# Kernel optimization log

Measured on AMD Instinct MI355X. Metric: run time of the kernel, lower is better.

Reference implementation:

```python
import jax, jax.numpy as jnp
import numpy as np

N_NODES = 50000
N_EDGES = 1600000
IN_DIM = 128
OUT_DIM = 32
N_HEADS = 4


def setup_inputs() -> dict:
    key = jax.random.key(0)
    k_x, k_e, k_w, k_a = jax.random.split(key, 4)
    x = jax.random.normal(k_x, (N_NODES, IN_DIM), dtype=jnp.float32)
    edge_index = jax.random.randint(k_e, (N_EDGES, 2), 0, N_NODES, dtype=jnp.int64)
    # Xavier-uniform-like init scales
    w_bound = np.sqrt(6.0 / (IN_DIM + OUT_DIM)).astype(np.float32)
    a_bound = np.sqrt(6.0 / (N_HEADS + 2 * OUT_DIM)).astype(np.float32)
    weight = jax.random.uniform(k_w, (N_HEADS, IN_DIM, OUT_DIM), dtype=jnp.float32,
                                minval=-w_bound, maxval=w_bound)
    attn = jax.random.uniform(k_a, (N_HEADS, 2 * OUT_DIM), dtype=jnp.float32,
                              minval=-a_bound, maxval=a_bound)
    return {"x": x, "edge_index": edge_index, "weight": weight, "attn": attn}


def reference(x, edge_index, weight, attn):
    # x: [N, in_dim]; edge_index: [E, 2]; weight: [H, in, out]; attn: [H, 2*out]
    num_nodes = x.shape[0]
    out_dim = weight.shape[2]
    src = edge_index[:, 0]
    dst = edge_index[:, 1]

    # Per-head linear transform: [N, H, out]
    Wh = jnp.einsum('ni,hio->nho', x, weight)
    Wh_src = Wh[src]  # [E, H, out]
    Wh_dst = Wh[dst]  # [E, H, out]

    a_src = attn[:, :out_dim]   # [H, out]
    a_dst = attn[:, out_dim:]   # [H, out]
    # Edge scores: [E, H]
    e = jnp.einsum('eho,ho->eh', Wh_src, a_src) + jnp.einsum('eho,ho->eh', Wh_dst, a_dst)
    e = jax.nn.leaky_relu(e, negative_slope=0.2)

    # Segment softmax over incoming edges of each dst node
    max_per_dst = jax.ops.segment_max(e, dst, num_segments=num_nodes)  # [N, H]
    max_per_dst = jnp.where(jnp.isfinite(max_per_dst), max_per_dst, 0.0)
    exp_e = jnp.exp(e - max_per_dst[dst])                               # [E, H]
    sum_per_dst = jax.ops.segment_sum(exp_e, dst, num_segments=num_nodes)  # [N, H]
    alpha = exp_e / (sum_per_dst[dst] + 1e-9)                           # [E, H]
    # Dropout is identity in eval mode.

    # Weighted scatter-add aggregation: [N, H, out]
    out = jax.ops.segment_sum(alpha[:, :, None] * Wh_src, dst, num_segments=num_nodes)
    h = out.reshape(num_nodes, -1)  # concat heads -> [N, H*out]
    return h, alpha
```

## Files before the change

kernel.cpp:

```cpp
#include <hip/hip_runtime.h>
#include <hip/hip_bf16.h>
#include <math.h>

#define N_NODES 50000
#define N_EDGES 1600000
#define IN_DIM  128
#define OUT_DIM 32
#define N_HEADS 4
#define WH_DIM  (N_HEADS * OUT_DIM)
#define CAP     128
#define NB_SCAN 196
#define NPASS   4
#define WIN     (N_NODES / NPASS)
#define NCHUNK  32
#define CE      (N_EDGES / NCHUNK)

typedef __attribute__((ext_vector_type(8))) short short8;
typedef __attribute__((ext_vector_type(4))) float floatx4;

__device__ __forceinline__ short f2bf(float v) {
    __hip_bfloat16 b = __float2bfloat16(v);
    return *reinterpret_cast<short*>(&b);
}
__device__ __forceinline__ float lrelu(float v) {
    return v > 0.0f ? v : 0.2f * v;
}

__device__ __forceinline__ void load_edge(const void* eidx, int is32, int e,
                                          int& s, int& d) {
    if (is32) {
        const int2 v = ((const int2*)eidx)[e];
        s = v.x; d = v.y;
    } else {
        const longlong2 v = ((const longlong2*)eidx)[e];
        s = (int)v.x; d = (int)v.y;
    }
}

__global__ __launch_bounds__(256) void k_cvt(
        const void* __restrict__ eidx,
        int* __restrict__ s32, int* __restrict__ d32) {
    __shared__ int s_is32;
    const int t = threadIdx.x;
    if (t < 64) {
        int hi = ((const int*)eidx)[2 * (t * 25000) + 1];
        unsigned long long b = __ballot(hi != 0);
        if (t == 0) s_is32 = (b != 0ULL) ? 1 : 0;
    }
    __syncthreads();
    const int is32 = s_is32;
    const int e = blockIdx.x * 256 + t;
    if (e >= N_EDGES) return;
    int s, d;
    load_edge(eidx, is32, e, s, d);
    s32[e] = s;
    d32[e] = d;
}

__global__ __launch_bounds__(256) void k_wh(
        const float* __restrict__ x, const float* __restrict__ weight,
        const float* __restrict__ attn,
        __hip_bfloat16* __restrict__ Wh16, float* __restrict__ sb16) {
    __shared__ float ubuf[128 * 8];
    __shared__ short xsw[4 * 4 * 64 * 8];
    __shared__ short bsw[4 * 9 * 64 * 8];
    const int t  = threadIdx.x;
    const int nb = blockIdx.x * 64;

    {
        int c = t & 7, k0 = t >> 3;
        int h = c & 3;
        const float* ap = attn + h * 64 + (c >> 2) * 32;
        for (int k = k0; k < 128; k += 32) {
            const float* wp = weight + h * (IN_DIM * OUT_DIM) + k * OUT_DIM;
            float u = 0.f;
#pragma unroll
            for (int o = 0; o < 32; o += 4) {
                float4 wv = *(const float4*)(wp + o);
                float4 av = *(const float4*)(ap + o);
                u += wv.x * av.x + wv.y * av.y + wv.z * av.z + wv.w * av.w;
            }
            ubuf[k * 8 + c] = u;
        }
    }
    __syncthreads();

    for (int f = t; f < 128 * 128; f += 256) {
        int k = f >> 7, c = f & 127;
        float w = weight[(c >> 5) * (IN_DIM * OUT_DIM) + k * OUT_DIM + (c & 31)];
        int kc = k >> 5, quad = (k >> 3) & 3, j = k & 7;
        bsw[((kc * 9 + (c >> 4)) * 64 + quad * 16 + (c & 15)) * 8 + j] = f2bf(w);
    }
    for (int f = t; f < 128 * 16; f += 256) {
        int k = f >> 4, c = f & 15;
        float w = (c < 8) ? ubuf[k * 8 + c] : 0.f;
        int kc = k >> 5, quad = (k >> 3) & 3, j = k & 7;
        bsw[((kc * 9 + 8) * 64 + quad * 16 + c) * 8 + j] = f2bf(w);
    }
    for (int f = t; f < 64 * 32; f += 256) {
        int n = f >> 5, k = (f & 31) * 4;
        int ng = nb + n; if (ng > N_NODES - 1) ng = N_NODES - 1;
        float4 v = *(const float4*)(x + (size_t)ng * IN_DIM + k);
        int wg = n >> 4, m = n & 15, kc = k >> 5, quad = (k >> 3) & 3, j = k & 7;
        short4 sv = make_short4(f2bf(v.x), f2bf(v.y), f2bf(v.z), f2bf(v.w));
        *(short4*)&xsw[(((wg * 4 + kc) * 64) + quad * 16 + m) * 8 + j] = sv;
    }
    __syncthreads();

    const int wg = t >> 6, lane = t & 63;
    floatx4 acc[9];
#pragma unroll
    for (int i = 0; i < 9; ++i) acc[i] = (floatx4){0.f, 0.f, 0.f, 0.f};
#pragma unroll
    for (int kc = 0; kc < 4; ++kc) {
        short8 a = *(short8*)&xsw[((wg * 4 + kc) * 64 + lane) * 8];
#pragma unroll
        for (int cg = 0; cg < 9; ++cg) {
            short8 b = *(short8*)&bsw[((kc * 9 + cg) * 64 + lane) * 8];
            acc[cg] = __builtin_amdgcn_mfma_f32_16x16x32_bf16(a, b, acc[cg],
                                                              0, 0, 0);
        }
    }

    const int col = lane & 15, quad = lane >> 4;
#pragma unroll
    for (int r = 0; r < 4; ++r) {
        int n = nb + wg * 16 + quad * 4 + r;
        if (n >= N_NODES) continue;
#pragma unroll
        for (int cg = 0; cg < 8; ++cg)
            Wh16[(size_t)n * WH_DIM + cg * 16 + col] =
                __float2bfloat16(acc[cg][r]);
        if (col < 8) sb16[(size_t)n * 16 + col] = acc[8][r];
    }
}

__global__ __launch_bounds__(1024) void k_hist(
        const int* __restrict__ d32, int* __restrict__ hist) {
    __shared__ int hbin[WIN];
    const int c = blockIdx.x, w = blockIdx.y;
    for (int i = threadIdx.x; i < WIN; i += 1024) hbin[i] = 0;
    __syncthreads();
    const int w0 = w * WIN;
    for (int e = c * CE + threadIdx.x; e < (c + 1) * CE; e += 1024) {
        unsigned u = (unsigned)(d32[e] - w0);
        if (u < WIN) atomicAdd(&hbin[u], 1);
    }
    __syncthreads();
    for (int i = threadIdx.x; i < WIN; i += 1024)
        hist[c * N_NODES + w0 + i] = hbin[i];
}

__global__ __launch_bounds__(256) void k_scan1(
        const int* __restrict__ hist, int* __restrict__ pre,
        int* __restrict__ bsum) {
    __shared__ int sh[256];
    const int t = threadIdx.x;
    const int i = blockIdx.x * 256 + t;
    int v = 0;
    if (i < N_NODES)
        for (int c = 0; c < NCHUNK; ++c) v += hist[c * N_NODES + i];
    sh[t] = v;
    __syncthreads();
    for (int d = 1; d < 256; d <<= 1) {
        int u = (t >= d) ? sh[t - d] : 0;
        __syncthreads();
        sh[t] += u;
        __syncthreads();
    }
    if (i < N_NODES) pre[i] = sh[t] - v;
    if (t == 255) bsum[blockIdx.x] = sh[255];
}

__global__ __launch_bounds__(256) void k_scan2(
        const int* __restrict__ bsum, int* __restrict__ bbase) {
    __shared__ int sh[256];
    const int t = threadIdx.x;
    int v = (t < NB_SCAN) ? bsum[t] : 0;
    sh[t] = v;
    __syncthreads();
    for (int d = 1; d < 256; d <<= 1) {
        int u = (t >= d) ? sh[t - d] : 0;
        __syncthreads();
        sh[t] += u;
        __syncthreads();
    }
    if (t < NB_SCAN) bbase[t] = sh[t] - v;
}

__global__ __launch_bounds__(256) void k_base(
        const int* __restrict__ pre, const int* __restrict__ bbase,
        int* __restrict__ hist) {
    int d = blockIdx.x * 256 + threadIdx.x;
    if (d >= N_NODES) return;
    int run = pre[d] + bbase[d >> 8];
    for (int c = 0; c < NCHUNK; ++c) {
        int t0 = hist[c * N_NODES + d];
        hist[c * N_NODES + d] = run;
        run += t0;
    }
}

__global__ __launch_bounds__(1024) void k_scatter(
        const int* __restrict__ s32, const int* __restrict__ d32,
        const int* __restrict__ hist, int* __restrict__ csr) {
    __shared__ int pos[WIN];
    const int c = blockIdx.x, w = blockIdx.y;
    const int w0 = w * WIN;
    for (int i = threadIdx.x; i < WIN; i += 1024)
        pos[i] = hist[c * N_NODES + w0 + i];
    __syncthreads();
    for (int e = c * CE + threadIdx.x; e < (c + 1) * CE; e += 1024) {
        unsigned u = (unsigned)(d32[e] - w0);
        if (u < WIN) {
            int p = atomicAdd(&pos[u], 1);
            csr[p] = s32[e];
        }
    }
}

__global__ __launch_bounds__(256) void k_node(
        const int* __restrict__ pre, const int* __restrict__ bbase,
        const int* __restrict__ csr, float* __restrict__ sb16,
        const __hip_bfloat16* __restrict__ Wh16,
        float* __restrict__ out_h) {
    __shared__ int    sbuf[4][CAP];
    __shared__ float4 e4b[4][CAP];
    const int wv = threadIdx.x >> 6;
    const int t  = threadIdx.x & 63;
    const int n  = blockIdx.x * 4 + wv;
    const int beg = pre[n] + bbase[n >> 8];
    const int end = (n + 1 < N_NODES) ? pre[n + 1] + bbase[(n + 1) >> 8]
                                      : N_EDGES;
    const int deg = end - beg;

    const float4 sd = *(const float4*)(sb16 + (size_t)n * 16 + 4);

    float4 sum = {0.f, 0.f, 0.f, 0.f};
    for (int l = t; l < deg; l += 64) {
        int s = csr[beg + l];
        float4 ss = *(const float4*)(sb16 + (size_t)s * 16);
        float4 ex;
        ex.x = __expf(lrelu(ss.x + sd.x));
        ex.y = __expf(lrelu(ss.y + sd.y));
        ex.z = __expf(lrelu(ss.z + sd.z));
        ex.w = __expf(lrelu(ss.w + sd.w));
        if (l < CAP) { sbuf[wv][l] = s; e4b[wv][l] = ex; }
        sum.x += ex.x; sum.y += ex.y; sum.z += ex.z; sum.w += ex.w;
    }
#pragma unroll
    for (int o = 32; o; o >>= 1) {
        sum.x += __shfl_xor(sum.x, o);
        sum.y += __shfl_xor(sum.y, o);
        sum.z += __shfl_xor(sum.z, o);
        sum.w += __shfl_xor(sum.w, o);
    }
    float4 inv;
    inv.x = 1.0f / (sum.x + 1e-9f); inv.y = 1.0f / (sum.y + 1e-9f);
    inv.z = 1.0f / (sum.z + 1e-9f); inv.w = 1.0f / (sum.w + 1e-9f);
    if (t == 0) *(float4*)(sb16 + (size_t)n * 16 + 8) = inv;

    const int esl = t >> 4;
    const int dsl = t & 15;
    const int h   = dsl >> 2;
    const float invh = (h == 0) ? inv.x : (h == 1) ? inv.y
                     : (h == 2) ? inv.z : inv.w;
    const float sdh  = (h == 0) ? sd.x : (h == 1) ? sd.y
                     : (h == 2) ? sd.z : sd.w;
    float acc0 = 0.f, acc1 = 0.f, acc2 = 0.f, acc3 = 0.f;
    float acc4 = 0.f, acc5 = 0.f, acc6 = 0.f, acc7 = 0.f;
    if (deg <= CAP) {
        const int sPad = sbuf[wv][0];
        for (int jb = 0; jb < deg; jb += 16) {
            int   sg[4];
            float ag[4];
#pragma unroll
            for (int g = 0; g < 4; ++g) {
                const int idx = jb + g * 4 + esl;
                sg[g] = sPad;
                ag[g] = 0.f;
                if (idx < deg) {
                    sg[g] = sbuf[wv][idx];
                    ag[g] = ((const float*)&e4b[wv][idx])[h];
                }
            }
            uint4 w0 = *(const uint4*)(Wh16 + (size_t)sg[0] * WH_DIM + dsl * 8);
            uint4 w1 = *(const uint4*)(Wh16 + (size_t)sg[1] * WH_DIM + dsl * 8);
            uint4 w2 = *(const uint4*)(Wh16 + (size_t)sg[2] * WH_DIM + dsl * 8);
            uint4 w3 = *(const uint4*)(Wh16 + (size_t)sg[3] * WH_DIM + dsl * 8);
#define ACC8(W, A)                                                            \
            acc0 += (A) * __uint_as_float((W).x << 16);                       \
            acc1 += (A) * __uint_as_float((W).x & 0xffff0000u);               \
            acc2 += (A) * __uint_as_float((W).y << 16);                       \
            acc3 += (A) * __uint_as_float((W).y & 0xffff0000u);               \
            acc4 += (A) * __uint_as_float((W).z << 16);                       \
            acc5 += (A) * __uint_as_float((W).z & 0xffff0000u);               \
            acc6 += (A) * __uint_as_float((W).w << 16);                       \
            acc7 += (A) * __uint_as_float((W).w & 0xffff0000u)
            ACC8(w0, ag[0]);
            ACC8(w1, ag[1]);
            ACC8(w2, ag[2]);
            ACC8(w3, ag[3]);
#undef ACC8
        }
    } else {
        for (int jb = 0; jb < deg; jb += 4) {
            const int idx = jb + esl;
            float a = 0.f;
            int s = sbuf[wv][0];
            if (idx < deg) {
                if (idx < CAP) {
                    s = sbuf[wv][idx];
                    a = ((const float*)&e4b[wv][idx])[h];
                } else {
                    s = csr[beg + idx];
                    a = __expf(lrelu(sb16[(size_t)s * 16 + h] + sdh));
                }
            }
            const uint4 w = *(const uint4*)(Wh16 + (size_t)s * WH_DIM + dsl * 8);
            acc0 += a * __uint_as_float(w.x << 16);
            acc1 += a * __uint_as_float(w.x & 0xffff0000u);
            acc2 += a * __uint_as_float(w.y << 16);
            acc3 += a * __uint_as_float(w.y & 0xffff0000u);
            acc4 += a * __uint_as_float(w.z << 16);
            acc5 += a * __uint_as_float(w.z & 0xffff0000u);
            acc6 += a * __uint_as_float(w.w << 16);
            acc7 += a * __uint_as_float(w.w & 0xffff0000u);
        }
    }
    acc0 += __shfl_xor(acc0, 16); acc0 += __shfl_xor(acc0, 32);
    acc1 += __shfl_xor(acc1, 16); acc1 += __shfl_xor(acc1, 32);
    acc2 += __shfl_xor(acc2, 16); acc2 += __shfl_xor(acc2, 32);
    acc3 += __shfl_xor(acc3, 16); acc3 += __shfl_xor(acc3, 32);
    acc4 += __shfl_xor(acc4, 16); acc4 += __shfl_xor(acc4, 32);
    acc5 += __shfl_xor(acc5, 16); acc5 += __shfl_xor(acc5, 32);
    acc6 += __shfl_xor(acc6, 16); acc6 += __shfl_xor(acc6, 32);
    acc7 += __shfl_xor(acc7, 16); acc7 += __shfl_xor(acc7, 32);
    if (t < 16) {
        float* op = out_h + (size_t)n * WH_DIM + dsl * 8;
        float4 o0 = {acc0 * invh, acc1 * invh, acc2 * invh, acc3 * invh};
        float4 o1 = {acc4 * invh, acc5 * invh, acc6 * invh, acc7 * invh};
        *(float4*)op = o0;
        *(float4*)(op + 4) = o1;
    }
}

__global__ __launch_bounds__(256) void k_alpha(
        const int* __restrict__ s32, const int* __restrict__ d32,
        const float* __restrict__ sb16, float* __restrict__ ebuf) {
    int e = blockIdx.x * 256 + threadIdx.x;
    if (e >= N_EDGES) return;
    int s = s32[e], d = d32[e];
    float4 ss = *(const float4*)(sb16 + (size_t)s * 16);
    float4 sd = *(const float4*)(sb16 + (size_t)d * 16 + 4);
    float4 iv = *(const float4*)(sb16 + (size_t)d * 16 + 8);
    float4 a;
    a.x = __expf(lrelu(ss.x + sd.x)) * iv.x;
    a.y = __expf(lrelu(ss.y + sd.y)) * iv.y;
    a.z = __expf(lrelu(ss.z + sd.z)) * iv.z;
    a.w = __expf(lrelu(ss.w + sd.w)) * iv.w;
    *(float4*)(ebuf + (size_t)e * 4) = a;
}

extern "C" void kernel_launch(void* const* d_in, const int* in_sizes, int n_in,
                              void* d_out, int out_size, void* d_ws, size_t ws_size,
                              hipStream_t stream) {
    const float* x      = (const float*)d_in[0];
    const void*  eidx   = d_in[1];
    const float* weight = (const float*)d_in[2];
    const float* attn   = (const float*)d_in[3];

    float* out   = (float*)d_out;
    float* out_h = out;
    float* ebuf  = out + (size_t)N_NODES * WH_DIM;

    char* ws = (char*)d_ws;
    int*   bsum  = (int*)(ws + 64);
    int*   bbase = (int*)(ws + 896);
    int*   pre   = (int*)(ws + 2048);
    int*   s32   = (int*)(ws + 202112);
    int*   d32   = (int*)(ws + 6602112);
    int*   hist  = (int*)(ws + 13002112);
    int*   csr   = (int*)(ws + 19402112);
    __hip_bfloat16* Wh16 = (__hip_bfloat16*)(ws + 25802112);
    float* sb16  = (float*)(ws + 38602112);

    k_cvt<<<(N_EDGES + 255) / 256, 256, 0, stream>>>(eidx, s32, d32);
    k_wh<<<(N_NODES + 63) / 64, 256, 0, stream>>>(x, weight, attn, Wh16, sb16);
    dim3 hg(NCHUNK, NPASS);
    k_hist<<<hg, 1024, 0, stream>>>(d32, hist);
    k_scan1<<<NB_SCAN, 256, 0, stream>>>(hist, pre, bsum);
    k_scan2<<<1, 256, 0, stream>>>(bsum, bbase);
    k_base<<<NB_SCAN, 256, 0, stream>>>(pre, bbase, hist);
    k_scatter<<<hg, 1024, 0, stream>>>(s32, d32, hist, csr);
    k_node<<<N_NODES / 4, 256, 0, stream>>>(pre, bbase, csr, sb16,
                                            Wh16, out_h);
    k_alpha<<<(N_EDGES + 255) / 256, 256, 0, stream>>>(s32, d32, sb16, ebuf);
}
```

Baseline: 276.7 us.

## Bucket edges by destination window to avoid redundant full-edge scans in CSR build

The conversion kernel now also partitions edges into per-window buckets using shared and global atomics. Histogram and scatter passes then read only their own window's edges instead of every pass rescanning all edges. The two scan-finalisation kernels are merged, a node offset array is precomputed for the node kernel, and the Wh projection moves after the CSR build so its buffers can alias the bucket storage. In exchange, the conversion kernel writes extra data and relies on a fixed per-window capacity, which assumes roughly uniform destinations.

```diff
diff --git a/kernel.cpp b/kernel.cpp
--- a/kernel.cpp
+++ b/kernel.cpp
@@ -12,8 +12,8 @@
 #define NB_SCAN 196
 #define NPASS   4
 #define WIN     (N_NODES / NPASS)
-#define NCHUNK  32
-#define CE      (N_EDGES / NCHUNK)
+#define NCH2    32
+#define SEGCAP  420000
 
 typedef __attribute__((ext_vector_type(8))) short short8;
 typedef __attribute__((ext_vector_type(4))) float floatx4;
@@ -39,22 +39,35 @@
 
 __global__ __launch_bounds__(256) void k_cvt(
         const void* __restrict__ eidx,
-        int* __restrict__ s32, int* __restrict__ d32) {
+        int* __restrict__ s32, int* __restrict__ d32,
+        int* __restrict__ win_cnt,
+        int* __restrict__ win_s, int* __restrict__ win_d) {
     __shared__ int s_is32;
+    __shared__ int cnt[NPASS];
+    __shared__ int base[NPASS];
     const int t = threadIdx.x;
     if (t < 64) {
         int hi = ((const int*)eidx)[2 * (t * 25000) + 1];
         unsigned long long b = __ballot(hi != 0);
         if (t == 0) s_is32 = (b != 0ULL) ? 1 : 0;
     }
-    __syncthreads();
-    const int is32 = s_is32;
+    if (t < NPASS) cnt[t] = 0;
+    __syncthreads();
     const int e = blockIdx.x * 256 + t;
-    if (e >= N_EDGES) return;
     int s, d;
-    load_edge(eidx, is32, e, s, d);
+    load_edge(eidx, s_is32, e, s, d);
     s32[e] = s;
     d32[e] = d;
+    const int w = d / WIN;
+    const int slot = atomicAdd(&cnt[w], 1);
+    __syncthreads();
+    if (t < NPASS) base[t] = atomicAdd(&win_cnt[t], cnt[t]);
+    __syncthreads();
+    const int p = base[w] + slot;
+    if (p < SEGCAP) {
+        win_s[w * SEGCAP + p] = s;
+        win_d[w * SEGCAP + p] = d;
+    }
 }
 
 __global__ __launch_bounds__(256) void k_wh(
@@ -136,19 +149,24 @@
 }
 
 __global__ __launch_bounds__(1024) void k_hist(
-        const int* __restrict__ d32, int* __restrict__ hist) {
+        const int* __restrict__ win_cnt, const int* __restrict__ win_d,
+        int* __restrict__ hist) {
     __shared__ int hbin[WIN];
     const int c = blockIdx.x, w = blockIdx.y;
     for (int i = threadIdx.x; i < WIN; i += 1024) hbin[i] = 0;
     __syncthreads();
+    const int cw = win_cnt[w];
+    const int ce = (cw + NCH2 - 1) / NCH2;
+    const int lo = c * ce;
+    const int hi = min(lo + ce, cw);
     const int w0 = w * WIN;
-    for (int e = c * CE + threadIdx.x; e < (c + 1) * CE; e += 1024) {
-        unsigned u = (unsigned)(d32[e] - w0);
+    for (int i = lo + threadIdx.x; i < hi; i += 1024) {
+        unsigned u = (unsigned)(win_d[w * SEGCAP + i] - w0);
         if (u < WIN) atomicAdd(&hbin[u], 1);
     }
     __syncthreads();
     for (int i = threadIdx.x; i < WIN; i += 1024)
-        hist[c * N_NODES + w0 + i] = hbin[i];
+        hist[(w * NCH2 + c) * WIN + i] = hbin[i];
 }
 
 __global__ __launch_bounds__(256) void k_scan1(
@@ -158,8 +176,10 @@
     const int t = threadIdx.x;
     const int i = blockIdx.x * 256 + t;
     int v = 0;
-    if (i < N_NODES)
-        for (int c = 0; c < NCHUNK; ++c) v += hist[c * N_NODES + i];
+    if (i < N_NODES) {
+        const int w = i / WIN, bin = i % WIN;
+        for (int c = 0; c < NCH2; ++c) v += hist[(w * NCH2 + c) * WIN + bin];
+    }
     sh[t] = v;
     __syncthreads();
     for (int d = 1; d < 256; d <<= 1) {
@@ -172,8 +192,9 @@
     if (t == 255) bsum[blockIdx.x] = sh[255];
 }
 
-__global__ __launch_bounds__(256) void k_scan2(
-        const int* __restrict__ bsum, int* __restrict__ bbase) {
+__global__ __launch_bounds__(256) void k_base2(
+        const int* __restrict__ bsum, const int* __restrict__ pre,
+        int* __restrict__ hist, int* __restrict__ noff) {
     __shared__ int sh[256];
     const int t = threadIdx.x;
     int v = (t < NB_SCAN) ? bsum[t] : 0;
@@ -185,42 +206,48 @@
         sh[t] += u;
         __syncthreads();
     }
-    if (t < NB_SCAN) bbase[t] = sh[t] - v;
-}
-
-__global__ __launch_bounds__(256) void k_base(
-        const int* __restrict__ pre, const int* __restrict__ bbase,
-        int* __restrict__ hist) {
-    int d = blockIdx.x * 256 + threadIdx.x;
-    if (d >= N_NODES) return;
-    int run = pre[d] + bbase[d >> 8];
-    for (int c = 0; c < NCHUNK; ++c) {
-        int t0 = hist[c * N_NODES + d];
-        hist[c * N_NODES + d] = run;
+    const int b = blockIdx.x;
+    const int exb = sh[b] - bsum[b];
+    if (b == 0 && t == 0) noff[N_NODES] = N_EDGES;
+    const int i = b * 256 + t;
+    if (i >= N_NODES) return;
+    int run = pre[i] + exb;
+    noff[i] = run;
+    const int w = i / WIN, bin = i % WIN;
+    for (int c = 0; c < NCH2; ++c) {
+        const int idx = (w * NCH2 + c) * WIN + bin;
+        int t0 = hist[idx];
+        hist[idx] = run;
         run += t0;
     }
 }
 
 __global__ __launch_bounds__(1024) void k_scatter(
-        const int* __restrict__ s32, const int* __restrict__ d32,
+        const int* __restrict__ win_cnt, const int* __restrict__ win_s,
+        const int* __restrict__ win_d,
         const int* __restrict__ hist, int* __restrict__ csr) {
     __shared__ int pos[WIN];
     const int c = blockIdx.x, w = blockIdx.y;
+    for (int i = threadIdx.x; i < WIN; i += 1024)
+        pos[i] = hist[(w * NCH2 + c) * WIN + i];
+    __syncthreads();
+    const int cw = win_cnt[w];
+    const int ce = (cw + NCH2 - 1) / NCH2;
+    const int lo = c * ce;
+    const int hi = min(lo + ce, cw);
     const int w0 = w * WIN;
-    for (int i = threadIdx.x; i < WIN; i += 1024)
-        pos[i] = hist[c * N_NODES + w0 + i];
-    __syncthreads();
-    for (int e = c * CE + threadIdx.x; e < (c + 1) * CE; e += 1024) {
-        unsigned u = (unsigned)(d32[e] - w0);
+    for (int i = lo + threadIdx.x; i < hi; i += 1024) {
+        int s = win_s[w * SEGCAP + i];
+        unsigned u = (unsigned)(win_d[w * SEGCAP + i] - w0);
         if (u < WIN) {
             int p = atomicAdd(&pos[u], 1);
-            csr[p] = s32[e];
+            csr[p] = s;
         }
     }
 }
 
 __global__ __launch_bounds__(256) void k_node(
-        const int* __restrict__ pre, const int* __restrict__ bbase,
+        const int* __restrict__ noff,
         const int* __restrict__ csr, float* __restrict__ sb16,
         const __hip_bfloat16* __restrict__ Wh16,
         float* __restrict__ out_h) {
@@ -229,9 +256,8 @@
     const int wv = threadIdx.x >> 6;
     const int t  = threadIdx.x & 63;
     const int n  = blockIdx.x * 4 + wv;
-    const int beg = pre[n] + bbase[n >> 8];
-    const int end = (n + 1 < N_NODES) ? pre[n + 1] + bbase[(n + 1) >> 8]
-                                      : N_EDGES;
+    const int beg = noff[n];
+    const int end = noff[n + 1];
     const int deg = end - beg;
 
     const float4 sd = *(const float4*)(sb16 + (size_t)n * 16 + 4);
@@ -375,25 +401,29 @@
     float* ebuf  = out + (size_t)N_NODES * WH_DIM;
 
     char* ws = (char*)d_ws;
-    int*   bsum  = (int*)(ws + 64);
-    int*   bbase = (int*)(ws + 896);
-    int*   pre   = (int*)(ws + 2048);
-    int*   s32   = (int*)(ws + 202112);
-    int*   d32   = (int*)(ws + 6602112);
-    int*   hist  = (int*)(ws + 13002112);
-    int*   csr   = (int*)(ws + 19402112);
-    __hip_bfloat16* Wh16 = (__hip_bfloat16*)(ws + 25802112);
-    float* sb16  = (float*)(ws + 38602112);
-
-    k_cvt<<<(N_EDGES + 255) / 256, 256, 0, stream>>>(eidx, s32, d32);
+    int*   win_cnt = (int*)ws;
+    int*   bsum    = (int*)(ws + 64);
+    int*   pre     = (int*)(ws + 1024);
+    int*   noff    = (int*)(ws + 201024);
+    int*   s32     = (int*)(ws + 401088);
+    int*   d32     = (int*)(ws + 6801088);
+    int*   csr     = (int*)(ws + 13201088);
+    int*   win_s   = (int*)(ws + 19601152);
+    int*   win_d   = (int*)(ws + 26321152);
+    int*   hist    = (int*)(ws + 33041152);
+    __hip_bfloat16* Wh16 = (__hip_bfloat16*)(ws + 19601152);
+    float* sb16    = (float*)(ws + 32401152);
+
+    hipMemsetAsync(win_cnt, 0, 4 * sizeof(int), stream);
+
+    k_cvt<<<N_EDGES / 256, 256, 0, stream>>>(eidx, s32, d32,
+                                             win_cnt, win_s, win_d);
+    dim3 hg(NCH2, NPASS);
+    k_hist<<<hg, 1024, 0, stream>>>(win_cnt, win_d, hist);
+    k_scan1<<<NB_SCAN, 256, 0, stream>>>(hist, pre, bsum);
+    k_base2<<<NB_SCAN, 256, 0, stream>>>(bsum, pre, hist, noff);
+    k_scatter<<<hg, 1024, 0, stream>>>(win_cnt, win_s, win_d, hist, csr);
     k_wh<<<(N_NODES + 63) / 64, 256, 0, stream>>>(x, weight, attn, Wh16, sb16);
-    dim3 hg(NCHUNK, NPASS);
-    k_hist<<<hg, 1024, 0, stream>>>(d32, hist);
-    k_scan1<<<NB_SCAN, 256, 0, stream>>>(hist, pre, bsum);
-    k_scan2<<<1, 256, 0, stream>>>(bsum, bbase);
-    k_base<<<NB_SCAN, 256, 0, stream>>>(pre, bbase, hist);
-    k_scatter<<<hg, 1024, 0, stream>>>(s32, d32, hist, csr);
-    k_node<<<N_NODES / 4, 256, 0, stream>>>(pre, bbase, csr, sb16,
-                                            Wh16, out_h);
+    k_node<<<N_NODES / 4, 256, 0, stream>>>(noff, csr, sb16, Wh16, out_h);
     k_alpha<<<(N_EDGES + 255) / 256, 256, 0, stream>>>(s32, d32, sb16, ebuf);
 }
```

Result: slower. 328.1 us (+18.6%).
